# Optimization experiments

Hardware: AMD Instinct MI355X
Metric: run time of the kernel (lower is better)

Reference implementation:

```python
import jax, jax.numpy as jnp
import numpy as np

EMBED_DIM = 1024
HEAD_NUM = 16
HEAD_DIM = EMBED_DIM // HEAD_NUM
T, B, S = 2048, 4, 2048


def setup_inputs() -> dict:
    key = jax.random.key(0)
    ks = jax.random.split(key, 11)
    s = 0.02
    return {
        "query": jax.random.normal(ks[0], (T, B, EMBED_DIM), jnp.float32),
        "key": jax.random.normal(ks[1], (S, B, EMBED_DIM), jnp.float32),
        "value": jax.random.normal(ks[2], (S, B, EMBED_DIM), jnp.float32),
        "q_proj_weight": jax.random.normal(ks[3], (EMBED_DIM, EMBED_DIM), jnp.float32) * s,
        "k_proj_weight": jax.random.normal(ks[4], (EMBED_DIM, EMBED_DIM), jnp.float32) * s,
        "v_proj_weight": jax.random.normal(ks[5], (EMBED_DIM, EMBED_DIM), jnp.float32) * s,
        "in_proj_bias": jax.random.normal(ks[6], (3 * EMBED_DIM,), jnp.float32) * s,
        "bias_k": jax.random.normal(ks[7], (1, 1, EMBED_DIM), jnp.float32) * s,
        "bias_v": jax.random.normal(ks[8], (1, 1, EMBED_DIM), jnp.float32) * s,
        "out_proj_weight": jax.random.normal(ks[9], (EMBED_DIM, EMBED_DIM), jnp.float32) * s,
        "out_proj_bias": jax.random.normal(ks[10], (EMBED_DIM,), jnp.float32) * s,
    }


def reference(query, key, value, q_proj_weight, k_proj_weight, v_proj_weight,
              in_proj_bias, bias_k, bias_v, out_proj_weight, out_proj_bias):
    t, b, e = query.shape
    h, hd = HEAD_NUM, HEAD_DIM
    scaling = float(hd) ** -0.5
    # input projections (F.linear: x @ W.T + b)
    q = (query @ q_proj_weight.T + in_proj_bias[:e]) * scaling          # [T,B,E]
    k = key @ k_proj_weight.T + in_proj_bias[e:2 * e]                   # [S,B,E]
    v = value @ v_proj_weight.T + in_proj_bias[2 * e:]                  # [S,B,E]
    # append bias_k / bias_v token along the sequence dim
    k = jnp.concatenate([k, jnp.broadcast_to(bias_k, (1, b, e))], axis=0)  # [S+1,B,E]
    v = jnp.concatenate([v, jnp.broadcast_to(bias_v, (1, b, e))], axis=0)  # [S+1,B,E]
    # split heads: [L, B, E] -> [B*H, L, hd]
    q = q.reshape(t, b * h, hd).transpose(1, 0, 2)
    k = k.reshape(-1, b * h, hd).transpose(1, 0, 2)
    v = v.reshape(-1, b * h, hd).transpose(1, 0, 2)
    # full O(T*S) attention, as in the original bmm->softmax->bmm
    weights = jax.nn.softmax(jnp.einsum('nqd,nkd->nqk', q, k), axis=-1)  # [B*H,T,S+1]
    out = jnp.einsum('nqk,nkd->nqd', weights, v)                         # [B*H,T,hd]
    out = out.transpose(1, 0, 2).reshape(t, b, e)
    out = out @ out_proj_weight.T + out_proj_bias
    avg_weights = weights.sum(axis=1) / h                                # [B*H,S+1]
    return out, avg_weights
```

## Files before the change

### kernel.cpp

```cpp
#include <hip/hip_runtime.h>

#define T_DIM 2048
#define B_DIM 4
#define S_DIM 2048
#define E_DIM 1024
#define H_NUM 16
#define HD    64
#define NH    64
#define SP1   2049
#define SPAD  2112
#define NCHUNK 33

typedef short bf16x8 __attribute__((ext_vector_type(8)));
typedef float f32x4  __attribute__((ext_vector_type(4)));
typedef float f32x16 __attribute__((ext_vector_type(16)));
typedef unsigned int u32;

#define QSCALE 0.18033688011112042f

#if __has_builtin(__builtin_amdgcn_exp2f)
__device__ __forceinline__ float exp2_fast(float x) { return __builtin_amdgcn_exp2f(x); }
#else
__device__ __forceinline__ float exp2_fast(float x) { return __expf(x * 0.6931471805599453f); }
#endif

__device__ __forceinline__ unsigned short f2bf(float x) {
    union { float f; unsigned int u; } v; v.f = x;
    unsigned int r = v.u + 0x7FFFu + ((v.u >> 16) & 1u);
    return (unsigned short)(r >> 16);
}

__device__ __forceinline__ u32 cvtpk_bf16(float lo, float hi) {
    u32 r;
    asm("v_cvt_pk_bf16_f32 %0, %1, %2" : "=v"(r) : "v"(lo), "v"(hi));
    return r;
}
__device__ __forceinline__ void plswap(u32& a, u32& b) {
    asm("v_permlane32_swap_b32 %0, %1" : "+v"(a), "+v"(b));
}

__global__ __launch_bounds__(256)
void cvt_bf16_k(const float* __restrict__ src, short* __restrict__ dst, int n8)
{
    int i = blockIdx.x * 256 + threadIdx.x;
    if (i >= n8) return;
    const float4* s = reinterpret_cast<const float4*>(src) + (size_t)i * 2;
    float4 a = s[0], b = s[1];
    bf16x8 o;
    o[0] = (short)f2bf(a.x); o[1] = (short)f2bf(a.y);
    o[2] = (short)f2bf(a.z); o[3] = (short)f2bf(a.w);
    o[4] = (short)f2bf(b.x); o[5] = (short)f2bf(b.y);
    o[6] = (short)f2bf(b.z); o[7] = (short)f2bf(b.w);
    *(reinterpret_cast<bf16x8*>(dst) + i) = o;
}

template<int MODE>
__global__ __launch_bounds__(256)
void gemm_bf16(const short* __restrict__ A, const short* __restrict__ W,
               const float* __restrict__ bias, void* __restrict__ outp)
{
    __shared__ short As[128][72];
    __shared__ short Bs[128][72];
    const int bm = blockIdx.x, bn = blockIdx.y;
    const int tid = threadIdx.x;
    const int l = tid & 63, w = tid >> 6;
    const int wr = w >> 1, wc = w & 1;
    const int lr = l & 15, lg = l >> 4;

    f32x4 acc[4][4] = {};

    for (int k0 = 0; k0 < E_DIM; k0 += 64) {
#pragma unroll
        for (int it = 0; it < 4; ++it) {
            const int idx = it * 256 + tid;
            const int row = idx >> 3, cg = idx & 7;
            size_t asrc;
            if (MODE == 3) {
                const int m = bm * 128 + row;
                asrc = ((size_t)((m & 3) * 16 + (k0 >> 6)) * T_DIM + (m >> 2)) * HD + cg * 8;
            } else {
                asrc = (size_t)(bm * 128 + row) * E_DIM + k0 + cg * 8;
            }
            *reinterpret_cast<bf16x8*>(&As[row][cg * 8]) =
                *reinterpret_cast<const bf16x8*>(A + asrc);
            *reinterpret_cast<bf16x8*>(&Bs[row][cg * 8]) =
                *reinterpret_cast<const bf16x8*>(W + (size_t)(bn * 128 + row) * E_DIM + k0 + cg * 8);
        }
        __syncthreads();
#pragma unroll
        for (int c = 0; c < 2; ++c) {
            bf16x8 af[4], bf[4];
#pragma unroll
            for (int mi = 0; mi < 4; ++mi)
                af[mi] = *reinterpret_cast<const bf16x8*>(&As[wr * 64 + mi * 16 + lr][c * 32 + lg * 8]);
#pragma unroll
            for (int ni = 0; ni < 4; ++ni)
                bf[ni] = *reinterpret_cast<const bf16x8*>(&Bs[wc * 64 + ni * 16 + lr][c * 32 + lg * 8]);
#pragma unroll
            for (int mi = 0; mi < 4; ++mi)
#pragma unroll
                for (int ni = 0; ni < 4; ++ni)
                    acc[mi][ni] = __builtin_amdgcn_mfma_f32_16x16x32_bf16(
                        af[mi], bf[ni], acc[mi][ni], 0, 0, 0);
        }
        __syncthreads();
    }

#pragma unroll
    for (int mi = 0; mi < 4; ++mi)
#pragma unroll
        for (int ni = 0; ni < 4; ++ni) {
            const int colg = bn * 128 + wc * 64 + ni * 16 + lr;
            const float bv = bias[colg];
#pragma unroll
            for (int r = 0; r < 4; ++r) {
                const int m = bm * 128 + wr * 64 + mi * 16 + lg * 4 + r;
                float v = acc[mi][ni][r] + bv;
                if (MODE == 3) {
                    ((float*)outp)[(size_t)m * E_DIM + colg] = v;
                } else {
                    if (MODE == 0) v *= QSCALE;
                    const int seq = m >> 2, b = m & 3;
                    const int head = colg >> 6, d = colg & 63;
                    const int sd = (MODE == 0) ? T_DIM : SPAD;
                    ((short*)outp)[((size_t)(b * 16 + head) * sd + seq) * HD + d] = (short)f2bf(v);
                }
            }
        }
}

__global__ void fill_kv_pad(short* __restrict__ k_h, short* __restrict__ v_h,
                            const float* __restrict__ bias_k,
                            const float* __restrict__ bias_v)
{
    const int d   = threadIdx.x;
    const int row = S_DIM + blockIdx.x;
    const int n   = blockIdx.y;
    short bk = 0, bv = 0;
    if (row == S_DIM) {
        bk = (short)f2bf(bias_k[(n & 15) * HD + d]);
        bv = (short)f2bf(bias_v[(n & 15) * HD + d]);
    }
    const size_t idx = ((size_t)n * SPAD + row) * HD + d;
    k_h[idx] = bk;
    v_h[idx] = bv;
}

__global__ __launch_bounds__(256)
void attn_mfma(const short* __restrict__ q_h, const short* __restrict__ k_h,
               const short* __restrict__ v_h, short* __restrict__ o_h,
               float* __restrict__ m_arr, float* __restrict__ l_arr)
{
    __shared__ short Ks[64 * 64];
    __shared__ short Vt[64 * 64];
    char* KsB = (char*)Ks;
    char* VtB = (char*)Vt;

    const int n = blockIdx.y, q0 = blockIdx.x * 128;
    const int tid = threadIdx.x, l = tid & 63, w = tid >> 6;
    const int ql = l & 31;
    const int hi = l >> 5;
    const int qrow = q0 + w * 32 + ql;

    bf16x8 aq0, aq1, aq2, aq3;
    {
        const short* qp = q_h + ((size_t)n * T_DIM + qrow) * HD + hi * 8;
        aq0 = *(const bf16x8*)(qp);
        aq1 = *(const bf16x8*)(qp + 16);
        aq2 = *(const bf16x8*)(qp + 32);
        aq3 = *(const bf16x8*)(qp + 48);
    }

    float m_run = -1e30f, l_run = 0.f;
    f32x16 accA, accB;
#pragma unroll
    for (int r = 0; r < 16; ++r) { accA[r] = 0.f; accB[r] = 0.f; }

    for (int kc = 0; kc < NCHUNK; ++kc) {
        const int s0 = kc * 64;
#pragma unroll
        for (int it = 0; it < 2; ++it) {
            const int idx = it * 256 + tid;
            const int row = idx >> 3, cg = idx & 7;
            bf16x8 kv = *(const bf16x8*)(k_h + ((size_t)n * SPAD + s0 + row) * HD + cg * 8);
            *(bf16x8*)(KsB + row * 128 + ((cg * 16) ^ ((row & 7) << 4))) = kv;
        }
        {
            const int sp = tid & 31, d0 = (tid >> 5) * 8;
            const short* vp = v_h + ((size_t)n * SPAD + s0 + 2 * sp) * HD + d0;
            bf16x8 va = *(const bf16x8*)(vp);
            bf16x8 vb = *(const bf16x8*)(vp + HD);
#pragma unroll
            for (int j = 0; j < 8; ++j) {
                u32 pk = (u32)(unsigned short)va[j] | ((u32)(unsigned short)vb[j] << 16);
                const int d = d0 + j;
                *(u32*)(VtB + d * 128 + ((4 * sp) ^ ((d & 7) << 4))) = pk;
            }
        }
        __syncthreads();

        f32x16 sc0, sc1;
#pragma unroll
        for (int r = 0; r < 16; ++r) { sc0[r] = 0.f; sc1[r] = 0.f; }
        const int coff = (hi * 16) ^ ((ql & 7) << 4);
#pragma unroll
        for (int sl = 0; sl < 4; ++sl) {
            bf16x8 kf0 = *(const bf16x8*)(KsB + ql * 128        + ((sl * 32) ^ coff ^ 0) + (coff & 16 ? 0 : 0));
            bf16x8 kf1 = *(const bf16x8*)(KsB + (32 + ql) * 128 + (((sl * 32) + hi * 16) ^ ((ql & 7) << 4)));
            kf0 = *(const bf16x8*)(KsB + ql * 128 + (((sl * 32) + hi * 16) ^ ((ql & 7) << 4)));
            bf16x8 qf = (sl == 0) ? aq0 : (sl == 1) ? aq1 : (sl == 2) ? aq2 : aq3;
            sc0 = __builtin_amdgcn_mfma_f32_32x32x16_bf16(kf0, qf, sc0, 0, 0, 0);
            sc1 = __builtin_amdgcn_mfma_f32_32x32x16_bf16(kf1, qf, sc1, 0, 0, 0);
        }

        if (s0 + 64 > SP1) {
#pragma unroll
            for (int r = 0; r < 16; ++r) {
                const int key = (r & 3) + 8 * (r >> 2) + 4 * hi;
                if (s0 + key >= SP1)      sc0[r] = -1e30f;
                if (s0 + 32 + key >= SP1) sc1[r] = -1e30f;
            }
        }

        float mx = sc0[0];
#pragma unroll
        for (int r = 1; r < 16; ++r) mx = fmaxf(mx, sc0[r]);
#pragma unroll
        for (int r = 0; r < 16; ++r) mx = fmaxf(mx, sc1[r]);
        mx = fmaxf(mx, __shfl_xor(mx, 32));
        if (!__all(mx - m_run <= 8.0f)) {
            const float mnew = fmaxf(m_run, mx);
            const float fac = exp2_fast(m_run - mnew);
            l_run *= fac;
#pragma unroll
            for (int r = 0; r < 16; ++r) { accA[r] *= fac; accB[r] *= fac; }
            m_run = mnew;
        }
        float ps = 0.f;
        float p0[16], p1[16];
#pragma unroll
        for (int r = 0; r < 16; ++r) { p0[r] = exp2_fast(sc0[r] - m_run); ps += p0[r]; }
#pragma unroll
        for (int r = 0; r < 16; ++r) { p1[r] = exp2_fast(sc1[r] - m_run); ps += p1[r]; }
        ps += __shfl_xor(ps, 32);
        l_run += ps;

        union PF { u32 u[4]; bf16x8 v; };
        PF pf0, pf1, pf2, pf3;
        {
            u32 a0 = cvtpk_bf16(p0[0], p0[1]),   b0 = cvtpk_bf16(p0[4], p0[5]);   plswap(a0, b0);
            u32 a1 = cvtpk_bf16(p0[2], p0[3]),   b1 = cvtpk_bf16(p0[6], p0[7]);   plswap(a1, b1);
            u32 a2 = cvtpk_bf16(p0[8], p0[9]),   b2 = cvtpk_bf16(p0[12], p0[13]); plswap(a2, b2);
            u32 a3 = cvtpk_bf16(p0[10], p0[11]), b3 = cvtpk_bf16(p0[14], p0[15]); plswap(a3, b3);
            pf0.u[0] = a0; pf0.u[1] = a1; pf0.u[2] = b0; pf0.u[3] = b1;
            pf1.u[0] = a2; pf1.u[1] = a3; pf1.u[2] = b2; pf1.u[3] = b3;
            u32 c0 = cvtpk_bf16(p1[0], p1[1]),   d0 = cvtpk_bf16(p1[4], p1[5]);   plswap(c0, d0);
            u32 c1 = cvtpk_bf16(p1[2], p1[3]),   d1 = cvtpk_bf16(p1[6], p1[7]);   plswap(c1, d1);
            u32 c2 = cvtpk_bf16(p1[8], p1[9]),   d2 = cvtpk_bf16(p1[12], p1[13]); plswap(c2, d2);
            u32 c3 = cvtpk_bf16(p1[10], p1[11]), d3 = cvtpk_bf16(p1[14], p1[15]); plswap(c3, d3);
            pf2.u[0] = c0; pf2.u[1] = c1; pf2.u[2] = d0; pf2.u[3] = d1;
            pf3.u[0] = c2; pf3.u[1] = c3; pf3.u[2] = d2; pf3.u[3] = d3;
        }

#pragma unroll
        for (int ksl = 0; ksl < 4; ++ksl) {
            const int cb = ((ksl * 32) + hi * 16) ^ ((ql & 7) << 4);
            bf16x8 vf0 = *(const bf16x8*)(VtB + ql * 128 + cb);
            bf16x8 vf1 = *(const bf16x8*)(VtB + (32 + ql) * 128 + cb);
            const bf16x8 pv = (ksl == 0) ? pf0.v : (ksl == 1) ? pf1.v : (ksl == 2) ? pf2.v : pf3.v;
            accA = __builtin_amdgcn_mfma_f32_32x32x16_bf16(vf0, pv, accA, 0, 0, 0);
            accB = __builtin_amdgcn_mfma_f32_32x32x16_bf16(vf1, pv, accB, 0, 0, 0);
        }
        __syncthreads();
    }

    const float il = 1.0f / l_run;
    short* orow = o_h + ((size_t)n * T_DIM + qrow) * HD;
#pragma unroll
    for (int rq = 0; rq < 4; ++rq) {
        uint2 st;
        st.x = cvtpk_bf16(accA[rq * 4 + 0] * il, accA[rq * 4 + 1] * il);
        st.y = cvtpk_bf16(accA[rq * 4 + 2] * il, accA[rq * 4 + 3] * il);
        *(uint2*)(orow + rq * 8 + hi * 4) = st;
        uint2 st2;
        st2.x = cvtpk_bf16(accB[rq * 4 + 0] * il, accB[rq * 4 + 1] * il);
        st2.y = cvtpk_bf16(accB[rq * 4 + 2] * il, accB[rq * 4 + 3] * il);
        *(uint2*)(orow + 32 + rq * 8 + hi * 4) = st2;
    }
    if (hi == 0) {
        m_arr[n * T_DIM + qrow] = m_run;
        l_arr[n * T_DIM + qrow] = l_run;
    }
}

__global__ __launch_bounds__(256)
void colsum_mfma(const short* __restrict__ q_h, const short* __restrict__ k_h,
                 const float* __restrict__ m_arr, const float* __restrict__ l_arr,
                 float* __restrict__ avg_out)
{
    __shared__ short Qs[64][72];
    __shared__ float ms[64];
    __shared__ float li[64];

    const int n = blockIdx.y, s0 = blockIdx.x * 64;
    const int tid = threadIdx.x, l = tid & 63, w = tid >> 6;
    const int lr = l & 15, lg = l >> 4;

    bf16x8 ak[2];
#pragma unroll
    for (int c = 0; c < 2; ++c)
        ak[c] = *reinterpret_cast<const bf16x8*>(
            k_h + ((size_t)n * SPAD + s0 + w * 16 + lr) * HD + c * 32 + lg * 8);

    float csum[4] = {0.f, 0.f, 0.f, 0.f};

    for (int qo = 0; qo < T_DIM; qo += 64) {
#pragma unroll
        for (int it = 0; it < 2; ++it) {
            const int idx = it * 256 + tid;
            const int row = idx >> 3, cg = idx & 7;
            *reinterpret_cast<bf16x8*>(&Qs[row][cg * 8]) =
                *reinterpret_cast<const bf16x8*>(q_h + ((size_t)n * T_DIM + qo + row) * HD + cg * 8);
        }
        if (tid < 64) ms[tid] = m_arr[n * T_DIM + qo + tid];
        else if (tid < 128) li[tid - 64] = 1.0f / l_arr[n * T_DIM + qo + tid - 64];
        __syncthreads();
#pragma unroll
        for (int qt = 0; qt < 4; ++qt) {
            bf16x8 bq0 = *reinterpret_cast<const bf16x8*>(&Qs[qt * 16 + lr][lg * 8]);
            bf16x8 bq1 = *reinterpret_cast<const bf16x8*>(&Qs[qt * 16 + lr][32 + lg * 8]);
            f32x4 z = {0.f, 0.f, 0.f, 0.f};
            z = __builtin_amdgcn_mfma_f32_16x16x32_bf16(ak[0], bq0, z, 0, 0, 0);
            z = __builtin_amdgcn_mfma_f32_16x16x32_bf16(ak[1], bq1, z, 0, 0, 0);
            const float mq = ms[qt * 16 + lr];
            const float lq = li[qt * 16 + lr];
#pragma unroll
            for (int r = 0; r < 4; ++r)
                csum[r] += exp2_fast(z[r] - mq) * lq;
        }
        __syncthreads();
    }
#pragma unroll
    for (int r = 0; r < 4; ++r) {
        float v = csum[r];
        v += __shfl_xor(v, 1, 16);
        v += __shfl_xor(v, 2, 16);
        v += __shfl_xor(v, 4, 16);
        v += __shfl_xor(v, 8, 16);
        if (lr == 0) {
            const int key = s0 + w * 16 + lg * 4 + r;
            if (key < SP1) avg_out[(size_t)n * SP1 + key] = v * 0.0625f;
        }
    }
}

extern "C" void kernel_launch(void* const* d_in, const int* in_sizes, int n_in,
                              void* d_out, int out_size, void* d_ws, size_t ws_size,
                              hipStream_t stream)
{
    const float* query   = (const float*)d_in[0];
    const float* key     = (const float*)d_in[1];
    const float* value   = (const float*)d_in[2];
    const float* wq      = (const float*)d_in[3];
    const float* wk      = (const float*)d_in[4];
    const float* wv      = (const float*)d_in[5];
    const float* in_bias = (const float*)d_in[6];
    const float* bias_k  = (const float*)d_in[7];
    const float* bias_v  = (const float*)d_in[8];
    const float* wo      = (const float*)d_in[9];
    const float* out_b   = (const float*)d_in[10];
    float* out = (float*)d_out;

    const size_t NTOK = (size_t)T_DIM * B_DIM;
    short* qx  = (short*)d_ws;
    short* kx  = qx  + NTOK * E_DIM;
    short* vx  = kx  + NTOK * E_DIM;
    short* wqb = vx  + NTOK * E_DIM;
    short* wkb = wqb + (size_t)E_DIM * E_DIM;
    short* wvb = wkb + (size_t)E_DIM * E_DIM;
    short* wob = wvb + (size_t)E_DIM * E_DIM;
    short* q_h = wob + (size_t)E_DIM * E_DIM;
    short* k_h = q_h + (size_t)NH * T_DIM * HD;
    short* v_h = k_h + (size_t)NH * SPAD * HD;
    short* o_h = v_h + (size_t)NH * SPAD * HD;
    float* m_arr = (float*)(o_h + (size_t)NH * T_DIM * HD);
    float* l_arr = m_arr + (size_t)NH * T_DIM;

    const int n8_x = (int)(NTOK * E_DIM / 8);
    const int n8_w = E_DIM * E_DIM / 8;
    const dim3 blk(256);
    hipLaunchKernelGGL(cvt_bf16_k, dim3((n8_x + 255) / 256), blk, 0, stream, query, qx, n8_x);
    hipLaunchKernelGGL(cvt_bf16_k, dim3((n8_x + 255) / 256), blk, 0, stream, key,   kx, n8_x);
    hipLaunchKernelGGL(cvt_bf16_k, dim3((n8_x + 255) / 256), blk, 0, stream, value, vx, n8_x);
    hipLaunchKernelGGL(cvt_bf16_k, dim3((n8_w + 255) / 256), blk, 0, stream, wq, wqb, n8_w);
    hipLaunchKernelGGL(cvt_bf16_k, dim3((n8_w + 255) / 256), blk, 0, stream, wk, wkb, n8_w);
    hipLaunchKernelGGL(cvt_bf16_k, dim3((n8_w + 255) / 256), blk, 0, stream, wv, wvb, n8_w);
    hipLaunchKernelGGL(cvt_bf16_k, dim3((n8_w + 255) / 256), blk, 0, stream, wo, wob, n8_w);

    const dim3 gg(64, 8);
    hipLaunchKernelGGL((gemm_bf16<0>), gg, blk, 0, stream, qx, wqb, in_bias,             (void*)q_h);
    hipLaunchKernelGGL((gemm_bf16<1>), gg, blk, 0, stream, kx, wkb, in_bias + E_DIM,     (void*)k_h);
    hipLaunchKernelGGL((gemm_bf16<2>), gg, blk, 0, stream, vx, wvb, in_bias + 2 * E_DIM, (void*)v_h);
    hipLaunchKernelGGL(fill_kv_pad, dim3(SPAD - S_DIM, NH), dim3(64), 0, stream,
                       k_h, v_h, bias_k, bias_v);
    hipLaunchKernelGGL(attn_mfma, dim3(T_DIM / 128, NH), blk, 0, stream,
                       q_h, k_h, v_h, o_h, m_arr, l_arr);
    hipLaunchKernelGGL(colsum_mfma, dim3(NCHUNK, NH), blk, 0, stream,
                       q_h, k_h, m_arr, l_arr, out + (size_t)T_DIM * B_DIM * E_DIM);
    hipLaunchKernelGGL((gemm_bf16<3>), gg, blk, 0, stream, o_h, wob, out_b, (void*)out);
}
```

Baseline: 333.9 us.

## Fuse fp32->bf16 input conversion into GEMMs and double-buffer attention/colsum LDS

The three large activation-conversion kernels are removed; the projection GEMMs now read fp32 query/key/value directly and convert to bf16 while staging into shared memory, eliminating an extra round trip of about 100 MB through HBM. The attention and column-sum kernels switch to double-buffered LDS with register prefetch of the next K/V or Q tile, which removes one barrier per iteration and overlaps global loads with MFMA work. s_setprio hints are added around the MFMA sections. In exchange the GEMM A-load traffic doubles in bytes, and the extra LDS and registers may lower occupancy.

```diff
diff --git a/kernel.cpp b/kernel.cpp
--- a/kernel.cpp
+++ b/kernel.cpp
@@ -56,7 +56,7 @@
 
 template<int MODE>
 __global__ __launch_bounds__(256)
-void gemm_bf16(const short* __restrict__ A, const short* __restrict__ W,
+void gemm_bf16(const void* __restrict__ Ap, const short* __restrict__ W,
                const float* __restrict__ bias, void* __restrict__ outp)
 {
     __shared__ short As[128][72];
@@ -74,19 +74,26 @@
         for (int it = 0; it < 4; ++it) {
             const int idx = it * 256 + tid;
             const int row = idx >> 3, cg = idx & 7;
-            size_t asrc;
             if (MODE == 3) {
                 const int m = bm * 128 + row;
-                asrc = ((size_t)((m & 3) * 16 + (k0 >> 6)) * T_DIM + (m >> 2)) * HD + cg * 8;
+                const size_t asrc =
+                    ((size_t)((m & 3) * 16 + (k0 >> 6)) * T_DIM + (m >> 2)) * HD + cg * 8;
+                *reinterpret_cast<bf16x8*>(&As[row][cg * 8]) =
+                    *reinterpret_cast<const bf16x8*>((const short*)Ap + asrc);
             } else {
-                asrc = (size_t)(bm * 128 + row) * E_DIM + k0 + cg * 8;
+                const float* ap = (const float*)Ap + (size_t)(bm * 128 + row) * E_DIM + k0 + cg * 8;
+                const float4 a0 = *reinterpret_cast<const float4*>(ap);
+                const float4 a1 = *reinterpret_cast<const float4*>(ap + 4);
+                uint4 st;
+                st.x = cvtpk_bf16(a0.x, a0.y); st.y = cvtpk_bf16(a0.z, a0.w);
+                st.z = cvtpk_bf16(a1.x, a1.y); st.w = cvtpk_bf16(a1.z, a1.w);
+                *reinterpret_cast<uint4*>(&As[row][cg * 8]) = st;
             }
-            *reinterpret_cast<bf16x8*>(&As[row][cg * 8]) =
-                *reinterpret_cast<const bf16x8*>(A + asrc);
             *reinterpret_cast<bf16x8*>(&Bs[row][cg * 8]) =
                 *reinterpret_cast<const bf16x8*>(W + (size_t)(bn * 128 + row) * E_DIM + k0 + cg * 8);
         }
         __syncthreads();
+        __builtin_amdgcn_s_setprio(1);
 #pragma unroll
         for (int c = 0; c < 2; ++c) {
             bf16x8 af[4], bf[4];
@@ -103,6 +110,7 @@
                     acc[mi][ni] = __builtin_amdgcn_mfma_f32_16x16x32_bf16(
                         af[mi], bf[ni], acc[mi][ni], 0, 0, 0);
         }
+        __builtin_amdgcn_s_setprio(0);
         __syncthreads();
     }
 
@@ -151,16 +159,21 @@
                const short* __restrict__ v_h, short* __restrict__ o_h,
                float* __restrict__ m_arr, float* __restrict__ l_arr)
 {
-    __shared__ short Ks[64 * 64];
-    __shared__ short Vt[64 * 64];
-    char* KsB = (char*)Ks;
-    char* VtB = (char*)Vt;
+    __shared__ short KsD[2][64 * 64];
+    __shared__ short VtD[2][64 * 64];
 
     const int n = blockIdx.y, q0 = blockIdx.x * 128;
     const int tid = threadIdx.x, l = tid & 63, w = tid >> 6;
     const int ql = l & 31;
     const int hi = l >> 5;
     const int qrow = q0 + w * 32 + ql;
+
+    const int krow = tid >> 3, kcg = tid & 7;
+    const int kswz = (kcg * 16) ^ ((krow & 7) << 4);
+    const int sp = tid & 31, d0 = (tid >> 5) * 8;
+
+    const short* kbase = k_h + (size_t)n * SPAD * HD;
+    const short* vbase = v_h + (size_t)n * SPAD * HD;
 
     bf16x8 aq0, aq1, aq2, aq3;
     {
@@ -171,48 +184,58 @@
         aq3 = *(const bf16x8*)(qp + 48);
     }
 
+    bf16x8 pk0 = *(const bf16x8*)(kbase + (size_t)krow * HD + kcg * 8);
+    bf16x8 pk1 = *(const bf16x8*)(kbase + (size_t)(32 + krow) * HD + kcg * 8);
+    bf16x8 pv0 = *(const bf16x8*)(vbase + (size_t)(2 * sp) * HD + d0);
+    bf16x8 pv1 = *(const bf16x8*)(vbase + (size_t)(2 * sp + 1) * HD + d0);
+    {
+        char* KsB = (char*)KsD[0];
+        char* VtB = (char*)VtD[0];
+        *(bf16x8*)(KsB + krow * 128 + kswz) = pk0;
+        *(bf16x8*)(KsB + (32 + krow) * 128 + kswz) = pk1;
+#pragma unroll
+        for (int j = 0; j < 8; ++j) {
+            u32 pk = (u32)(unsigned short)pv0[j] | ((u32)(unsigned short)pv1[j] << 16);
+            const int d = d0 + j;
+            *(u32*)(VtB + d * 128 + ((4 * sp) ^ ((d & 7) << 4))) = pk;
+        }
+    }
+    __syncthreads();
+
     float m_run = -1e30f, l_run = 0.f;
     f32x16 accA, accB;
 #pragma unroll
     for (int r = 0; r < 16; ++r) { accA[r] = 0.f; accB[r] = 0.f; }
 
     for (int kc = 0; kc < NCHUNK; ++kc) {
-        const int s0 = kc * 64;
-#pragma unroll
-        for (int it = 0; it < 2; ++it) {
-            const int idx = it * 256 + tid;
-            const int row = idx >> 3, cg = idx & 7;
-            bf16x8 kv = *(const bf16x8*)(k_h + ((size_t)n * SPAD + s0 + row) * HD + cg * 8);
-            *(bf16x8*)(KsB + row * 128 + ((cg * 16) ^ ((row & 7) << 4))) = kv;
-        }
-        {
-            const int sp = tid & 31, d0 = (tid >> 5) * 8;
-            const short* vp = v_h + ((size_t)n * SPAD + s0 + 2 * sp) * HD + d0;
-            bf16x8 va = *(const bf16x8*)(vp);
-            bf16x8 vb = *(const bf16x8*)(vp + HD);
-#pragma unroll
-            for (int j = 0; j < 8; ++j) {
-                u32 pk = (u32)(unsigned short)va[j] | ((u32)(unsigned short)vb[j] << 16);
-                const int d = d0 + j;
-                *(u32*)(VtB + d * 128 + ((4 * sp) ^ ((d & 7) << 4))) = pk;
-            }
-        }
-        __syncthreads();
+        const char* KsB = (const char*)KsD[kc & 1];
+        const char* VtB = (const char*)VtD[kc & 1];
+        const bool more = (kc + 1 < NCHUNK);
+
+        if (more) {
+            const int s0n = (kc + 1) * 64;
+            pk0 = *(const bf16x8*)(kbase + (size_t)(s0n + krow) * HD + kcg * 8);
+            pk1 = *(const bf16x8*)(kbase + (size_t)(s0n + 32 + krow) * HD + kcg * 8);
+            pv0 = *(const bf16x8*)(vbase + (size_t)(s0n + 2 * sp) * HD + d0);
+            pv1 = *(const bf16x8*)(vbase + (size_t)(s0n + 2 * sp + 1) * HD + d0);
+        }
 
         f32x16 sc0, sc1;
 #pragma unroll
         for (int r = 0; r < 16; ++r) { sc0[r] = 0.f; sc1[r] = 0.f; }
-        const int coff = (hi * 16) ^ ((ql & 7) << 4);
+        __builtin_amdgcn_s_setprio(1);
 #pragma unroll
         for (int sl = 0; sl < 4; ++sl) {
-            bf16x8 kf0 = *(const bf16x8*)(KsB + ql * 128        + ((sl * 32) ^ coff ^ 0) + (coff & 16 ? 0 : 0));
-            bf16x8 kf1 = *(const bf16x8*)(KsB + (32 + ql) * 128 + (((sl * 32) + hi * 16) ^ ((ql & 7) << 4)));
-            kf0 = *(const bf16x8*)(KsB + ql * 128 + (((sl * 32) + hi * 16) ^ ((ql & 7) << 4)));
+            const int cb = ((sl * 32) + hi * 16) ^ ((ql & 7) << 4);
+            bf16x8 kf0 = *(const bf16x8*)(KsB + ql * 128 + cb);
+            bf16x8 kf1 = *(const bf16x8*)(KsB + (32 + ql) * 128 + cb);
             bf16x8 qf = (sl == 0) ? aq0 : (sl == 1) ? aq1 : (sl == 2) ? aq2 : aq3;
             sc0 = __builtin_amdgcn_mfma_f32_32x32x16_bf16(kf0, qf, sc0, 0, 0, 0);
             sc1 = __builtin_amdgcn_mfma_f32_32x32x16_bf16(kf1, qf, sc1, 0, 0, 0);
         }
-
+        __builtin_amdgcn_s_setprio(0);
+
+        const int s0 = kc * 64;
         if (s0 + 64 > SP1) {
 #pragma unroll
             for (int r = 0; r < 16; ++r) {
@@ -254,14 +277,15 @@
             u32 a3 = cvtpk_bf16(p0[10], p0[11]), b3 = cvtpk_bf16(p0[14], p0[15]); plswap(a3, b3);
             pf0.u[0] = a0; pf0.u[1] = a1; pf0.u[2] = b0; pf0.u[3] = b1;
             pf1.u[0] = a2; pf1.u[1] = a3; pf1.u[2] = b2; pf1.u[3] = b3;
-            u32 c0 = cvtpk_bf16(p1[0], p1[1]),   d0 = cvtpk_bf16(p1[4], p1[5]);   plswap(c0, d0);
-            u32 c1 = cvtpk_bf16(p1[2], p1[3]),   d1 = cvtpk_bf16(p1[6], p1[7]);   plswap(c1, d1);
-            u32 c2 = cvtpk_bf16(p1[8], p1[9]),   d2 = cvtpk_bf16(p1[12], p1[13]); plswap(c2, d2);
-            u32 c3 = cvtpk_bf16(p1[10], p1[11]), d3 = cvtpk_bf16(p1[14], p1[15]); plswap(c3, d3);
-            pf2.u[0] = c0; pf2.u[1] = c1; pf2.u[2] = d0; pf2.u[3] = d1;
-            pf3.u[0] = c2; pf3.u[1] = c3; pf3.u[2] = d2; pf3.u[3] = d3;
-        }
-
+            u32 c0 = cvtpk_bf16(p1[0], p1[1]),   d0_ = cvtpk_bf16(p1[4], p1[5]);   plswap(c0, d0_);
+            u32 c1 = cvtpk_bf16(p1[2], p1[3]),   d1_ = cvtpk_bf16(p1[6], p1[7]);   plswap(c1, d1_);
+            u32 c2 = cvtpk_bf16(p1[8], p1[9]),   d2_ = cvtpk_bf16(p1[12], p1[13]); plswap(c2, d2_);
+            u32 c3 = cvtpk_bf16(p1[10], p1[11]), d3_ = cvtpk_bf16(p1[14], p1[15]); plswap(c3, d3_);
+            pf2.u[0] = c0; pf2.u[1] = c1; pf2.u[2] = d0_; pf2.u[3] = d1_;
+            pf3.u[0] = c2; pf3.u[1] = c3; pf3.u[2] = d2_; pf3.u[3] = d3_;
+        }
+
+        __builtin_amdgcn_s_setprio(1);
 #pragma unroll
         for (int ksl = 0; ksl < 4; ++ksl) {
             const int cb = ((ksl * 32) + hi * 16) ^ ((ql & 7) << 4);
@@ -271,7 +295,21 @@
             accA = __builtin_amdgcn_mfma_f32_32x32x16_bf16(vf0, pv, accA, 0, 0, 0);
             accB = __builtin_amdgcn_mfma_f32_32x32x16_bf16(vf1, pv, accB, 0, 0, 0);
         }
-        __syncthreads();
+        __builtin_amdgcn_s_setprio(0);
+
+        if (more) {
+            char* KsN = (char*)KsD[(kc & 1) ^ 1];
+            char* VtN = (char*)VtD[(kc & 1) ^ 1];
+            *(bf16x8*)(KsN + krow * 128 + kswz) = pk0;
+            *(bf16x8*)(KsN + (32 + krow) * 128 + kswz) = pk1;
+#pragma unroll
+            for (int j = 0; j < 8; ++j) {
+                u32 pk = (u32)(unsigned short)pv0[j] | ((u32)(unsigned short)pv1[j] << 16);
+                const int d = d0 + j;
+                *(u32*)(VtN + d * 128 + ((4 * sp) ^ ((d & 7) << 4))) = pk;
+            }
+            __syncthreads();
+        }
     }
 
     const float il = 1.0f / l_run;
@@ -298,13 +336,16 @@
                  const float* __restrict__ m_arr, const float* __restrict__ l_arr,
                  float* __restrict__ avg_out)
 {
-    __shared__ short Qs[64][72];
-    __shared__ float ms[64];
-    __shared__ float li[64];
+    __shared__ short Qs[2][64][72];
+    __shared__ float msh[2][64];
+    __shared__ float lih[2][64];
 
     const int n = blockIdx.y, s0 = blockIdx.x * 64;
     const int tid = threadIdx.x, l = tid & 63, w = tid >> 6;
     const int lr = l & 15, lg = l >> 4;
+    const int qr = tid >> 3, qcg = tid & 7;
+
+    const short* qbase = q_h + (size_t)n * T_DIM * HD;
 
     bf16x8 ak[2];
 #pragma unroll
@@ -312,34 +353,53 @@
         ak[c] = *reinterpret_cast<const bf16x8*>(
             k_h + ((size_t)n * SPAD + s0 + w * 16 + lr) * HD + c * 32 + lg * 8);
 
+    bf16x8 qa = *(const bf16x8*)(qbase + (size_t)qr * HD + qcg * 8);
+    bf16x8 qb = *(const bf16x8*)(qbase + (size_t)(32 + qr) * HD + qcg * 8);
+    float mlv = 0.f;
+    if (tid < 64) mlv = m_arr[n * T_DIM + tid];
+    else if (tid < 128) mlv = l_arr[n * T_DIM + tid - 64];
+    *(bf16x8*)&Qs[0][qr][qcg * 8] = qa;
+    *(bf16x8*)&Qs[0][32 + qr][qcg * 8] = qb;
+    if (tid < 64) msh[0][tid] = mlv;
+    else if (tid < 128) lih[0][tid - 64] = 1.0f / mlv;
+    __syncthreads();
+
     float csum[4] = {0.f, 0.f, 0.f, 0.f};
 
-    for (int qo = 0; qo < T_DIM; qo += 64) {
-#pragma unroll
-        for (int it = 0; it < 2; ++it) {
-            const int idx = it * 256 + tid;
-            const int row = idx >> 3, cg = idx & 7;
-            *reinterpret_cast<bf16x8*>(&Qs[row][cg * 8]) =
-                *reinterpret_cast<const bf16x8*>(q_h + ((size_t)n * T_DIM + qo + row) * HD + cg * 8);
-        }
-        if (tid < 64) ms[tid] = m_arr[n * T_DIM + qo + tid];
-        else if (tid < 128) li[tid - 64] = 1.0f / l_arr[n * T_DIM + qo + tid - 64];
-        __syncthreads();
+    for (int it = 0; it < T_DIM / 64; ++it) {
+        const int buf = it & 1;
+        const bool more = (it + 1 < T_DIM / 64);
+        if (more) {
+            const int qo = (it + 1) * 64;
+            qa = *(const bf16x8*)(qbase + (size_t)(qo + qr) * HD + qcg * 8);
+            qb = *(const bf16x8*)(qbase + (size_t)(qo + 32 + qr) * HD + qcg * 8);
+            if (tid < 64) mlv = m_arr[n * T_DIM + qo + tid];
+            else if (tid < 128) mlv = l_arr[n * T_DIM + qo + tid - 64];
+        }
+        __builtin_amdgcn_s_setprio(1);
 #pragma unroll
         for (int qt = 0; qt < 4; ++qt) {
-            bf16x8 bq0 = *reinterpret_cast<const bf16x8*>(&Qs[qt * 16 + lr][lg * 8]);
-            bf16x8 bq1 = *reinterpret_cast<const bf16x8*>(&Qs[qt * 16 + lr][32 + lg * 8]);
+            bf16x8 bq0 = *reinterpret_cast<const bf16x8*>(&Qs[buf][qt * 16 + lr][lg * 8]);
+            bf16x8 bq1 = *reinterpret_cast<const bf16x8*>(&Qs[buf][qt * 16 + lr][32 + lg * 8]);
             f32x4 z = {0.f, 0.f, 0.f, 0.f};
             z = __builtin_amdgcn_mfma_f32_16x16x32_bf16(ak[0], bq0, z, 0, 0, 0);
             z = __builtin_amdgcn_mfma_f32_16x16x32_bf16(ak[1], bq1, z, 0, 0, 0);
-            const float mq = ms[qt * 16 + lr];
-            const float lq = li[qt * 16 + lr];
+            const float mq = msh[buf][qt * 16 + lr];
+            const float lq = lih[buf][qt * 16 + lr];
 #pragma unroll
             for (int r = 0; r < 4; ++r)
                 csum[r] += exp2_fast(z[r] - mq) * lq;
         }
-        __syncthreads();
-    }
+        __builtin_amdgcn_s_setprio(0);
+        if (more) {
+            *(bf16x8*)&Qs[buf ^ 1][qr][qcg * 8] = qa;
+            *(bf16x8*)&Qs[buf ^ 1][32 + qr][qcg * 8] = qb;
+            if (tid < 64) msh[buf ^ 1][tid] = mlv;
+            else if (tid < 128) lih[buf ^ 1][tid - 64] = 1.0f / mlv;
+            __syncthreads();
+        }
+    }
+
 #pragma unroll
     for (int r = 0; r < 4; ++r) {
         float v = csum[r];
@@ -371,11 +431,7 @@
     const float* out_b   = (const float*)d_in[10];
     float* out = (float*)d_out;
 
-    const size_t NTOK = (size_t)T_DIM * B_DIM;
-    short* qx  = (short*)d_ws;
-    short* kx  = qx  + NTOK * E_DIM;
-    short* vx  = kx  + NTOK * E_DIM;
-    short* wqb = vx  + NTOK * E_DIM;
+    short* wqb = (short*)d_ws;
     short* wkb = wqb + (size_t)E_DIM * E_DIM;
     short* wvb = wkb + (size_t)E_DIM * E_DIM;
     short* wob = wvb + (size_t)E_DIM * E_DIM;
@@ -386,26 +442,22 @@
     float* m_arr = (float*)(o_h + (size_t)NH * T_DIM * HD);
     float* l_arr = m_arr + (size_t)NH * T_DIM;
 
-    const int n8_x = (int)(NTOK * E_DIM / 8);
     const int n8_w = E_DIM * E_DIM / 8;
     const dim3 blk(256);
-    hipLaunchKernelGGL(cvt_bf16_k, dim3((n8_x + 255) / 256), blk, 0, stream, query, qx, n8_x);
-    hipLaunchKernelGGL(cvt_bf16_k, dim3((n8_x + 255) / 256), blk, 0, stream, key,   kx, n8_x);
-    hipLaunchKernelGGL(cvt_bf16_k, dim3((n8_x + 255) / 256), blk, 0, stream, value, vx, n8_x);
     hipLaunchKernelGGL(cvt_bf16_k, dim3((n8_w + 255) / 256), blk, 0, stream, wq, wqb, n8_w);
     hipLaunchKernelGGL(cvt_bf16_k, dim3((n8_w + 255) / 256), blk, 0, stream, wk, wkb, n8_w);
     hipLaunchKernelGGL(cvt_bf16_k, dim3((n8_w + 255) / 256), blk, 0, stream, wv, wvb, n8_w);
     hipLaunchKernelGGL(cvt_bf16_k, dim3((n8_w + 255) / 256), blk, 0, stream, wo, wob, n8_w);
 
     const dim3 gg(64, 8);
-    hipLaunchKernelGGL((gemm_bf16<0>), gg, blk, 0, stream, qx, wqb, in_bias,             (void*)q_h);
-    hipLaunchKernelGGL((gemm_bf16<1>), gg, blk, 0, stream, kx, wkb, in_bias + E_DIM,     (void*)k_h);
-    hipLaunchKernelGGL((gemm_bf16<2>), gg, blk, 0, stream, vx, wvb, in_bias + 2 * E_DIM, (void*)v_h);
+    hipLaunchKernelGGL((gemm_bf16<0>), gg, blk, 0, stream, (const void*)query, wqb, in_bias,             (void*)q_h);
+    hipLaunchKernelGGL((gemm_bf16<1>), gg, blk, 0, stream, (const void*)key,   wkb, in_bias + E_DIM,     (void*)k_h);
+    hipLaunchKernelGGL((gemm_bf16<2>), gg, blk, 0, stream, (const void*)value, wvb, in_bias + 2 * E_DIM, (void*)v_h);
     hipLaunchKernelGGL(fill_kv_pad, dim3(SPAD - S_DIM, NH), dim3(64), 0, stream,
                        k_h, v_h, bias_k, bias_v);
     hipLaunchKernelGGL(attn_mfma, dim3(T_DIM / 128, NH), blk, 0, stream,
                        q_h, k_h, v_h, o_h, m_arr, l_arr);
     hipLaunchKernelGGL(colsum_mfma, dim3(NCHUNK, NH), blk, 0, stream,
                        q_h, k_h, m_arr, l_arr, out + (size_t)T_DIM * B_DIM * E_DIM);
-    hipLaunchKernelGGL((gemm_bf16<3>), gg, blk, 0, stream, o_h, wob, out_b, (void*)out);
-}
+    hipLaunchKernelGGL((gemm_bf16<3>), gg, blk, 0, stream, (const void*)o_h, wob, out_b, (void*)out);
+}
```

Result: faster. 303.5 us (-9.1%).
